# Kernel optimization log

Hardware: AMD Instinct MI355X
Metric: run time of the kernel (lower is better)

The kernel has to match this reference:

```python
import jax, jax.numpy as jnp
import numpy as np

V = 32000   # target_vocab_size
E = 512     # embedding_dim
L = 2       # enc_lstm_layers
HD = 512    # enc_lstm_hidden_dim (bidirectional encoder)
H = 2 * HD  # decoder LSTM hidden size
B = 16
T = 128
BOS = 1
CTX = L * 2 * HD          # stepwise context dim = 2048
IN0 = E + CTX             # decoder LSTM layer-0 input dim = 2560


def setup_inputs() -> dict:
    key = jax.random.key(0)
    ks = jax.random.split(key, 12)
    def w(k, shape, fan_in):
        return jax.random.normal(k, shape, jnp.float32) * np.float32(1.0 / np.sqrt(fan_in))
    return {
        "enc_lstm_hidden": jax.random.normal(ks[0], (2 * L, B, HD), jnp.float32),
        "enc_lstm_ctxt": jax.random.normal(ks[1], (2 * L, B, HD), jnp.float32),
        "minibatch_target": jax.random.randint(ks[2], (B, T), 0, V, dtype=jnp.int32),
        "emb": w(ks[3], (V, E), E),
        "w_ih_0": w(ks[4], (4 * H, IN0), IN0),
        "w_hh_0": w(ks[5], (4 * H, H), H),
        "b_ih_0": jnp.zeros((4 * H,), jnp.float32),
        "b_hh_0": jnp.zeros((4 * H,), jnp.float32),
        "w_ih_1": w(ks[6], (4 * H, H), H),
        "w_hh_1": w(ks[7], (4 * H, H), H),
        "b_ih_1": jnp.zeros((4 * H,), jnp.float32),
        "b_hh_1": jnp.zeros((4 * H,), jnp.float32),
        "fc_w": w(ks[8], (V, H), H),
        "fc_b": jnp.zeros((V,), jnp.float32),
    }


def _lstm_layer(x_seq, h0, c0, w_ih, w_hh, b):
    """x_seq: [T, B, in]; returns top outputs [T, B, H]. torch gate order i,f,g,o."""
    def step(carry, x):
        h, c = carry
        g = x @ w_ih.T + h @ w_hh.T + b
        i, f, gg, o = jnp.split(g, 4, axis=-1)
        c = jax.nn.sigmoid(f) * c + jax.nn.sigmoid(i) * jnp.tanh(gg)
        h = jax.nn.sigmoid(o) * jnp.tanh(c)
        return (h, c), h
    (hT, cT), ys = jax.lax.scan(step, (h0, c0), x_seq)
    return ys, hT, cT


def reference(enc_lstm_hidden, enc_lstm_ctxt, minibatch_target, emb,
              w_ih_0, w_hh_0, b_ih_0, b_hh_0,
              w_ih_1, w_hh_1, b_ih_1, b_hh_1, fc_w, fc_b):
    # _reshape_encoder_state: [2L,B,HD] -> [L,B,2HD] (interleave fwd/bwd per layer)
    def reshape_state(s):
        return s.reshape(L, 2, B, HD).transpose(0, 2, 1, 3).reshape(L, B, 2 * HD)
    h0 = reshape_state(enc_lstm_hidden)
    c0 = reshape_state(enc_lstm_ctxt)
    # stepwise input context: [B, 2L*HD]
    ctx = jnp.transpose(enc_lstm_hidden, (1, 0, 2)).reshape(B, CTX)
    # teacher forcing: prev tokens = [BOS, target[:, :-1]]
    tokens = jnp.concatenate(
        [jnp.full((B, 1), BOS, minibatch_target.dtype), minibatch_target[:, :-1]], axis=1)
    tok_emb = emb[tokens]                                   # [B,T,E]
    ctx_b = jnp.broadcast_to(ctx[:, None, :], (B, T, CTX))  # [B,T,CTX]
    x = jnp.concatenate([tok_emb, ctx_b], axis=-1).transpose(1, 0, 2)  # [T,B,IN0]
    x, _, _ = _lstm_layer(x, h0[0], c0[0], w_ih_0, w_hh_0, b_ih_0 + b_hh_0)
    x, _, _ = _lstm_layer(x, h0[1], c0[1], w_ih_1, w_hh_1, b_ih_1 + b_hh_1)
    out = jnp.tanh(x)                                       # [T,B,H]
    logits = jnp.einsum('tbh,vh->btv', out, fc_w) + fc_b    # [B,T,V]
    return logits
```

## Files before the change

kernel.cpp:

```cpp
#include <hip/hip_runtime.h>


#define NBLK 128

typedef float f32x4 __attribute__((ext_vector_type(4)));
typedef __bf16 bf16x8 __attribute__((ext_vector_type(8)));
typedef unsigned short u16;

__device__ __forceinline__ float sigf(float x) { return 1.0f / (1.0f + __expf(-x)); }
__device__ __forceinline__ float tanh_(float x) {
  x = fminf(15.0f, fmaxf(-15.0f, x));
  float e = __expf(2.0f * x);
  return (e - 1.0f) / (e + 1.0f);
}

__device__ __forceinline__ u16 f2bf(float f) {
  __bf16 h = (__bf16)f;
  return __builtin_bit_cast(u16, h);
}

__device__ __forceinline__ bf16x8 cvt8(float4 a, float4 b) {
  bf16x8 v;
  v[0] = (__bf16)a.x; v[1] = (__bf16)a.y; v[2] = (__bf16)a.z; v[3] = (__bf16)a.w;
  v[4] = (__bf16)b.x; v[5] = (__bf16)b.y; v[6] = (__bf16)b.z; v[7] = (__bf16)b.w;
  return v;
}

__device__ __forceinline__ void st_cv16(u16* p, u16 v) {
  unsigned vv = v;
  asm volatile("global_store_short %0, %1, off sc0 sc1" :: "v"(p), "v"(vv) : "memory");
}

__device__ __forceinline__ void flag_store(unsigned* p, unsigned v) {
  asm volatile("global_store_dword %0, %1, off sc0 sc1" :: "v"(p), "v"(v) : "memory");
}

__device__ __forceinline__ void ld2_flags(const unsigned* p0, const unsigned* p1,
                                          unsigned& a, unsigned& b) {
  asm volatile(
      "global_load_dword %0, %2, off sc0 sc1\n\t"
      "global_load_dword %1, %3, off sc0 sc1\n\t"
      "s_waitcnt vmcnt(0)"
      : "=&v"(a), "=&v"(b)
      : "v"(p0), "v"(p1)
      : "memory");
}

__device__ __forceinline__ void gsyncf(unsigned step, unsigned* bar) {
  asm volatile("s_waitcnt vmcnt(0)" ::: "memory");
  __syncthreads();
  const int tid = threadIdx.x;
  if (tid == 0) flag_store(bar + 32 + blockIdx.x * 32, step);
  if (tid < 64) {
    const unsigned* p0 = bar + 32 + tid * 64;
    const unsigned* p1 = p0 + 32;
    for (;;) {
      unsigned a, b;
      ld2_flags(p0, p1, a, b);
      if (__all((a >= step) & (b >= step))) break;
      __builtin_amdgcn_s_sleep(1);
    }
    asm volatile("" ::: "memory");
  }
  __syncthreads();
}

__device__ __forceinline__ void dot4(float& a, float4 wv, float4 xv) {
  a = fmaf(wv.x, xv.x, a);
  a = fmaf(wv.y, xv.y, a);
  a = fmaf(wv.z, xv.z, a);
  a = fmaf(wv.w, xv.w, a);
}

__global__ void prep_emb(const int* __restrict__ tgt, const float* __restrict__ emb,
                         u16* __restrict__ x0b) {
  const int g = blockIdx.x * blockDim.x + threadIdx.x;
  const int col8 = (g & 63) * 8;
  const int tb = g >> 6;
  const int t = tb >> 4, b = tb & 15;
  const int tok = (t == 0) ? 1 : tgt[b * 128 + (t - 1)];
  const float* s = emb + (size_t)tok * 512 + col8;
  float4 a = *(const float4*)s;
  float4 bb = *(const float4*)(s + 4);
  __align__(16) u16 r[8] = {f2bf(a.x), f2bf(a.y), f2bf(a.z), f2bf(a.w),
                            f2bf(bb.x), f2bf(bb.y), f2bf(bb.z), f2bf(bb.w)};
  *(uint4*)(x0b + (size_t)tb * 512 + col8) = *(uint4*)r;
}

__global__ __launch_bounds__(256, 1) void prep_ctx(const float* __restrict__ enc_h,
                                                   const float* __restrict__ wih0,
                                                   float* __restrict__ cp) {
  __shared__ float ctx[16][2052];
  const int tid = threadIdx.x;
#pragma unroll
  for (int c = 0; c < 32; ++c) {
    int f4 = tid + c * 256;
    int b = f4 >> 9, kq = f4 & 511;
    *(float4*)&ctx[b][kq * 4] =
        *(const float4*)(enc_h + (kq >> 7) * 8192 + b * 512 + (kq & 127) * 4);
  }
  __syncthreads();
  const int jr = tid >> 4, b = tid & 15;
  const int j = blockIdx.x * 16 + jr;
  const float* w = wih0 + (size_t)j * 2560 + 512;
  float a0 = 0.f, a1 = 0.f, a2 = 0.f, a3 = 0.f;
  for (int k = 0; k < 2048; k += 16) {
    float4 w0 = *(const float4*)(w + k);
    float4 w1 = *(const float4*)(w + k + 4);
    float4 w2 = *(const float4*)(w + k + 8);
    float4 w3 = *(const float4*)(w + k + 12);
    float4 x0 = *(const float4*)&ctx[b][k];
    float4 x1 = *(const float4*)&ctx[b][k + 4];
    float4 x2 = *(const float4*)&ctx[b][k + 8];
    float4 x3 = *(const float4*)&ctx[b][k + 12];
    dot4(a0, w0, x0); dot4(a1, w1, x1); dot4(a2, w2, x2); dot4(a3, w3, x3);
  }
  cp[(size_t)j * 16 + b] = a0 + a1 + a2 + a3;
}

#define BURST(ACC, BP, S, XOFF, BW)                                            \
  _Pragma("unroll")                                                            \
  for (int mm = 0; mm < 16; ++mm) {                                            \
    bf16x8 av = *(const bf16x8*)&(BP)[fr * (S) + (XOFF) + mm * 32 + ks8];      \
    ACC = __builtin_amdgcn_mfma_f32_16x16x32_bf16(av, (BW)[mm], ACC, 0, 0, 0); \
  }

__device__ __forceinline__ void loadw(bf16x8* dst, int q, int w8, int lane,
                                      const float* wih0, const float* whh0,
                                      const float* wih1, const float* whh1) {
  const int c = q >> 1, tile = q & 1;
  const int nn = lane & 15;
  const int gate = tile * 2 + (nn >> 3);
  const int unit = nn & 7;
  const int j = gate * 1024 + w8 + unit;
  const float* src;
  size_t stride = 1024;
  int ko = 0;
  if (c == 0) { src = wih0; stride = 2560; ko = 0; }
  else if (c <= 2) { src = whh0; ko = (c - 1) * 512; }
  else if (c <= 4) { src = wih1; ko = (c - 3) * 512; }
  else { src = whh1; ko = (c - 5) * 512; }
  const float* base = src + (size_t)j * stride + ko + ((lane >> 4) * 8);
#pragma unroll
  for (int mm = 0; mm < 16; ++mm) {
    const float* sp = base + mm * 32;
    dst[mm] = cvt8(*(const float4*)sp, *(const float4*)(sp + 4));
  }
}

__global__ __launch_bounds__(512, 2) void dec_seq_rw2(
    const float* __restrict__ enc_h, const float* __restrict__ enc_c,
    const float* __restrict__ wih0, const float* __restrict__ whh0,
    const float* __restrict__ wih1, const float* __restrict__ whh1,
    const float* __restrict__ bih0, const float* __restrict__ bhh0,
    const float* __restrict__ bih1, const float* __restrict__ bhh1,
    const float* __restrict__ cp, const u16* __restrict__ x0b,
    u16* __restrict__ xr, u16* __restrict__ h1r,
    u16* __restrict__ out2b, unsigned* bar) {
  __shared__ u16 xe[16 * 520];
  __shared__ u16 xs[16 * 1032];
  __shared__ u16 h1s[16 * 1032];
  __shared__ float gls[14][16][17];

  const int tid = threadIdx.x;
  const int wgid = blockIdx.x;
  const int w8 = wgid * 8;
  const int lane = tid & 63;
  const int wave = tid >> 6;
  const int fr = lane & 15;
  const int ks8 = (lane >> 4) * 8;
  unsigned step = 0;

  bf16x8 bw0[16], bw1[16];
  const int q0 = (wave < 6) ? 2 * wave : (wave == 6 ? 12 : 13);
  loadw(bw0, q0, w8, lane, wih0, whh0, wih1, whh1);
  if (wave < 6) loadw(bw1, 2 * wave + 1, w8, lane, wih0, whh0, wih1, whh1);
  else {
#pragma unroll
    for (int mm = 0; mm < 16; ++mm) bw1[mm] = bf16x8{};
  }

  const int gdj = (tid >> 4) & 7;
  const int gb = tid & 15;
  float cpA0 = 0.f, cpA1 = 0.f, cpA2 = 0.f, cpA3 = 0.f;
  float cpB0 = 0.f, cpB1 = 0.f, cpB2 = 0.f, cpB3 = 0.f;
  float c0r = 0.f, c1r = 0.f;
  if (tid < 128) {
    const int jp = w8 + gdj;
    cpA0 = cp[(size_t)(jp) * 16 + gb] + bih0[jp] + bhh0[jp];
    cpA1 = cp[(size_t)(1024 + jp) * 16 + gb] + bih0[1024 + jp] + bhh0[1024 + jp];
    cpA2 = cp[(size_t)(2048 + jp) * 16 + gb] + bih0[2048 + jp] + bhh0[2048 + jp];
    cpA3 = cp[(size_t)(3072 + jp) * 16 + gb] + bih0[3072 + jp] + bhh0[3072 + jp];
    cpB0 = bih1[jp] + bhh1[jp];
    cpB1 = bih1[1024 + jp] + bhh1[1024 + jp];
    cpB2 = bih1[2048 + jp] + bhh1[2048 + jp];
    cpB3 = bih1[3072 + jp] + bhh1[3072 + jp];
    const int dir = jp >> 9, e = jp & 511;
    c0r = enc_c[dir * 8192 + gb * 512 + e];
    c1r = enc_c[(2 + dir) * 8192 + gb * 512 + e];
    st_cv16(xr + gb * 1024 + jp, f2bf(enc_h[dir * 8192 + gb * 512 + e]));
    st_cv16(h1r + gb * 1024 + jp, f2bf(enc_h[(2 + dir) * 8192 + gb * 512 + e]));
  }

  const int sm = tid >> 5;
  const int skq = (tid & 31) * 8;

  {
    const u16* se = x0b + sm * 512;
#pragma unroll
    for (int jj = 0; jj < 2; ++jj)
      *(uint4*)&xe[sm * 520 + skq + jj * 256] = *(const uint4*)(se + skq + jj * 256);
  }
  gsyncf(++step, bar);

  for (int s = 0; s < 129; ++s) {
    const bool doA = (s < 128), doB = (s >= 1);

    uint4 rx[4], rh[4] = {}, re[2] = {};
    {
      const u16* sx = xr + (size_t)s * 16384 + sm * 1024;
#pragma unroll
      for (int jj = 0; jj < 4; ++jj) rx[jj] = *(const uint4*)(sx + skq + jj * 256);
      if (doB) {
        const u16* sh = h1r + (size_t)(s - 1) * 16384 + sm * 1024;
#pragma unroll
        for (int jj = 0; jj < 4; ++jj) rh[jj] = *(const uint4*)(sh + skq + jj * 256);
      }
      if (s < 127) {
        const u16* se = x0b + (size_t)(s + 1) * 8192 + sm * 512;
#pragma unroll
        for (int jj = 0; jj < 2; ++jj) re[jj] = *(const uint4*)(se + skq + jj * 256);
      }
    }
#pragma unroll
    for (int jj = 0; jj < 4; ++jj) *(uint4*)&xs[sm * 1032 + skq + jj * 256] = rx[jj];
    if (doB) {
#pragma unroll
      for (int jj = 0; jj < 4; ++jj) *(uint4*)&h1s[sm * 1032 + skq + jj * 256] = rh[jj];
    }
    __syncthreads();

    f32x4 acc0 = {0.f, 0.f, 0.f, 0.f}, acc1 = {0.f, 0.f, 0.f, 0.f};
    bool act0 = false, act1 = false;
    if (wave == 0) { if (doA) { BURST(acc0, xe, 520, 0, bw0) BURST(acc1, xe, 520, 0, bw1) act0 = act1 = true; } }
    else if (wave == 1) { if (doA) { BURST(acc0, xs, 1032, 0, bw0) BURST(acc1, xs, 1032, 0, bw1) act0 = act1 = true; } }
    else if (wave == 2) { if (doA) { BURST(acc0, xs, 1032, 512, bw0) BURST(acc1, xs, 1032, 512, bw1) act0 = act1 = true; } }
    else if (wave == 3) { if (doB) { BURST(acc0, xs, 1032, 0, bw0) BURST(acc1, xs, 1032, 0, bw1) act0 = act1 = true; } }
    else if (wave == 4) { if (doB) { BURST(acc0, xs, 1032, 512, bw0) BURST(acc1, xs, 1032, 512, bw1) act0 = act1 = true; } }
    else if (wave == 5) { if (doB) { BURST(acc0, h1s, 1032, 0, bw0) BURST(acc1, h1s, 1032, 0, bw1) act0 = act1 = true; } }
    else if (wave == 6) { if (doB) { BURST(acc0, h1s, 1032, 512, bw0) act0 = true; } }
    else { if (doB) { BURST(acc0, h1s, 1032, 512, bw0) act0 = true; } }
    if (act0) {
#pragma unroll
      for (int r = 0; r < 4; ++r) gls[q0][fr][(lane >> 4) * 4 + r] = acc0[r];
    }
    if (act1) {
#pragma unroll
      for (int r = 0; r < 4; ++r) gls[q0 + 1][fr][(lane >> 4) * 4 + r] = acc1[r];
    }
    __syncthreads();

    if (s < 127) {
#pragma unroll
      for (int jj = 0; jj < 2; ++jj) *(uint4*)&xe[sm * 520 + skq + jj * 256] = re[jj];
    }

    if (tid < 128) {
      const int jp = w8 + gdj;
      if (doA) {
        float gi = gls[0][gdj][gb] + gls[2][gdj][gb] + gls[4][gdj][gb] + cpA0;
        float gf = gls[0][8 + gdj][gb] + gls[2][8 + gdj][gb] + gls[4][8 + gdj][gb] + cpA1;
        float gg = gls[1][gdj][gb] + gls[3][gdj][gb] + gls[5][gdj][gb] + cpA2;
        float go = gls[1][8 + gdj][gb] + gls[3][8 + gdj][gb] + gls[5][8 + gdj][gb] + cpA3;
        c0r = sigf(gf) * c0r + sigf(gi) * tanh_(gg);
        float h = sigf(go) * tanh_(c0r);
        st_cv16(xr + (size_t)(s + 1) * 16384 + gb * 1024 + jp, f2bf(h));
      }
      if (doB) {
        float gi = gls[6][gdj][gb] + gls[8][gdj][gb] + gls[10][gdj][gb] +
                   gls[12][gdj][gb] + cpB0;
        float gf = gls[6][8 + gdj][gb] + gls[8][8 + gdj][gb] + gls[10][8 + gdj][gb] +
                   gls[12][8 + gdj][gb] + cpB1;
        float gg = gls[7][gdj][gb] + gls[9][gdj][gb] + gls[11][gdj][gb] +
                   gls[13][gdj][gb] + cpB2;
        float go = gls[7][8 + gdj][gb] + gls[9][8 + gdj][gb] + gls[11][8 + gdj][gb] +
                   gls[13][8 + gdj][gb] + cpB3;
        c1r = sigf(gf) * c1r + sigf(gi) * tanh_(gg);
        float h = sigf(go) * tanh_(c1r);
        st_cv16(h1r + (size_t)s * 16384 + gb * 1024 + jp, f2bf(h));
        out2b[((s - 1) * 16 + gb) * 1024 + jp] = f2bf(tanh_(h));
      }
    }
    gsyncf(++step, bar);
  }
}

__global__ __launch_bounds__(256, 2) void fc_gemm_mfma(
    const u16* __restrict__ A, const float* __restrict__ Bw,
    const float* __restrict__ bias, float* __restrict__ C) {
  __shared__ __align__(16) u16 Al[128][40];
  __shared__ __align__(16) u16 Bl[128][40];

  const int tid = threadIdx.x;
  const int m0 = blockIdx.x * 128;
  const int n0 = blockIdx.y * 128;
  const int wave = tid >> 6;
  const int lane = tid & 63;
  const int wm = (wave & 1) * 64;
  const int wn = (wave >> 1) * 64;
  const int fr = lane & 15;
  const int ks = lane >> 4;

  const int srow = tid >> 1;
  const int sh16 = (tid & 1) * 16;

  const u16* Ag = A + (size_t)(m0 + srow) * 1024 + sh16;
  const float* Bg = Bw + (size_t)(n0 + srow) * 1024 + sh16;

  f32x4 acc[4][4] = {};

  for (int k0 = 0; k0 < 1024; k0 += 32) {
    uint4 a0 = *(const uint4*)(Ag + k0);
    uint4 a1 = *(const uint4*)(Ag + k0 + 8);
    float bfv[16];
    *(float4*)&bfv[0] = *(const float4*)(Bg + k0);
    *(float4*)&bfv[4] = *(const float4*)(Bg + k0 + 4);
    *(float4*)&bfv[8] = *(const float4*)(Bg + k0 + 8);
    *(float4*)&bfv[12] = *(const float4*)(Bg + k0 + 12);
    u16 bu[16];
#pragma unroll
    for (int u = 0; u < 16; ++u) bu[u] = f2bf(bfv[u]);

    __syncthreads();
    *(uint4*)&Al[srow][sh16] = a0;
    *(uint4*)&Al[srow][sh16 + 8] = a1;
    *(uint4*)&Bl[srow][sh16] = *(uint4*)&bu[0];
    *(uint4*)&Bl[srow][sh16 + 8] = *(uint4*)&bu[8];
    __syncthreads();

    bf16x8 af[4], bf[4];
#pragma unroll
    for (int i = 0; i < 4; ++i) af[i] = *(const bf16x8*)&Al[wm + i * 16 + fr][ks * 8];
#pragma unroll
    for (int j = 0; j < 4; ++j) bf[j] = *(const bf16x8*)&Bl[wn + j * 16 + fr][ks * 8];
#pragma unroll
    for (int i = 0; i < 4; ++i)
#pragma unroll
      for (int j = 0; j < 4; ++j)
        acc[i][j] = __builtin_amdgcn_mfma_f32_16x16x32_bf16(af[i], bf[j], acc[i][j], 0, 0, 0);
  }

  float bj[4];
#pragma unroll
  for (int j = 0; j < 4; ++j) bj[j] = bias[n0 + wn + j * 16 + fr];

  const int mrb = (lane >> 4) * 4;
#pragma unroll
  for (int i = 0; i < 4; ++i) {
#pragma unroll
    for (int r = 0; r < 4; ++r) {
      const int m = m0 + wm + i * 16 + mrb + r;
      float* dst = C + ((size_t)(m & 15) * 128 + (m >> 4)) * 32000;
#pragma unroll
      for (int j = 0; j < 4; ++j) {
        dst[n0 + wn + j * 16 + fr] = acc[i][j][r] + bj[j];
      }
    }
  }
}

extern "C" void kernel_launch(void* const* d_in, const int* in_sizes, int n_in,
                              void* d_out, int out_size, void* d_ws, size_t ws_size,
                              hipStream_t stream) {
  const float* enc_h = (const float*)d_in[0];
  const float* enc_c = (const float*)d_in[1];
  const int* tgt = (const int*)d_in[2];
  const float* emb = (const float*)d_in[3];
  const float* wih0 = (const float*)d_in[4];
  const float* whh0 = (const float*)d_in[5];
  const float* bih0 = (const float*)d_in[6];
  const float* bhh0 = (const float*)d_in[7];
  const float* wih1 = (const float*)d_in[8];
  const float* whh1 = (const float*)d_in[9];
  const float* bih1 = (const float*)d_in[10];
  const float* bhh1 = (const float*)d_in[11];
  const float* fcw = (const float*)d_in[12];
  const float* fcb = (const float*)d_in[13];
  float* logits = (float*)d_out;

  unsigned* bar = (unsigned*)d_ws;
  hipMemsetAsync(d_ws, 0, 32768, stream);

  float* cp = (float*)((char*)d_ws + 32768);
  u16* x0b = (u16*)(cp + 65536);
  u16* xr = x0b + 1048576;
  u16* h1r = xr + 2113536;
  u16* out2b = h1r + 2113536;

  prep_emb<<<512, 256, 0, stream>>>(tgt, emb, x0b);
  prep_ctx<<<256, 256, 0, stream>>>(enc_h, wih0, cp);
  dec_seq_rw2<<<NBLK, 512, 0, stream>>>(enc_h, enc_c, wih0, whh0, wih1, whh1,
                                        bih0, bhh0, bih1, bhh1, cp, x0b,
                                        xr, h1r, out2b, bar);
  fc_gemm_mfma<<<dim3(16, 250), 256, 0, stream>>>(out2b, fcw, fcb, logits);
}
```

Before: 1.048 ms.

## Pre-convert FC weights to bf16 once per call and restructure context projection

Adds a kernel that converts fc_w to bf16 in workspace before the decoder runs. The FC GEMM then loads bf16 weights directly instead of converting fp32 in every one of the 16 M-tiles, which cuts redundant global reads and conversion work. prep_ctx is rewritten so each 16-lane group splits K and reuses each weight float4 across all 16 batch rows, followed by a shuffle reduction. The bf16 path only runs when the workspace is large enough, and the extra conversion pass adds its own traffic.

```diff
diff --git a/kernel.cpp b/kernel.cpp
--- a/kernel.cpp
+++ b/kernel.cpp
@@ -72,6 +72,15 @@
   a = fmaf(wv.w, xv.w, a);
 }
 
+__global__ void prep_bf16(const float* __restrict__ src, u16* __restrict__ dst, int n8) {
+  for (int i = blockIdx.x * blockDim.x + threadIdx.x; i < n8; i += gridDim.x * blockDim.x) {
+    float4 a = *(const float4*)(src + (size_t)i * 8);
+    float4 b = *(const float4*)(src + (size_t)i * 8 + 4);
+    bf16x8 v = cvt8(a, b);
+    *(uint4*)(dst + (size_t)i * 8) = __builtin_bit_cast(uint4, v);
+  }
+}
+
 __global__ void prep_emb(const int* __restrict__ tgt, const float* __restrict__ emb,
                          u16* __restrict__ x0b) {
   const int g = blockIdx.x * blockDim.x + threadIdx.x;
@@ -82,14 +91,13 @@
   const float* s = emb + (size_t)tok * 512 + col8;
   float4 a = *(const float4*)s;
   float4 bb = *(const float4*)(s + 4);
-  __align__(16) u16 r[8] = {f2bf(a.x), f2bf(a.y), f2bf(a.z), f2bf(a.w),
-                            f2bf(bb.x), f2bf(bb.y), f2bf(bb.z), f2bf(bb.w)};
-  *(uint4*)(x0b + (size_t)tb * 512 + col8) = *(uint4*)r;
-}
-
-__global__ __launch_bounds__(256, 1) void prep_ctx(const float* __restrict__ enc_h,
-                                                   const float* __restrict__ wih0,
-                                                   float* __restrict__ cp) {
+  bf16x8 v = cvt8(a, bb);
+  *(uint4*)(x0b + (size_t)tb * 512 + col8) = __builtin_bit_cast(uint4, v);
+}
+
+__global__ __launch_bounds__(256, 1) void prep_ctx2(const float* __restrict__ enc_h,
+                                                    const float* __restrict__ wih0,
+                                                    float* __restrict__ cp) {
   __shared__ float ctx[16][2052];
   const int tid = threadIdx.x;
 #pragma unroll
@@ -100,22 +108,22 @@
         *(const float4*)(enc_h + (kq >> 7) * 8192 + b * 512 + (kq & 127) * 4);
   }
   __syncthreads();
-  const int jr = tid >> 4, b = tid & 15;
-  const int j = blockIdx.x * 16 + jr;
+  const int r = tid >> 4, l = tid & 15;
+  const int j = blockIdx.x * 16 + r;
   const float* w = wih0 + (size_t)j * 2560 + 512;
-  float a0 = 0.f, a1 = 0.f, a2 = 0.f, a3 = 0.f;
-  for (int k = 0; k < 2048; k += 16) {
-    float4 w0 = *(const float4*)(w + k);
-    float4 w1 = *(const float4*)(w + k + 4);
-    float4 w2 = *(const float4*)(w + k + 8);
-    float4 w3 = *(const float4*)(w + k + 12);
-    float4 x0 = *(const float4*)&ctx[b][k];
-    float4 x1 = *(const float4*)&ctx[b][k + 4];
-    float4 x2 = *(const float4*)&ctx[b][k + 8];
-    float4 x3 = *(const float4*)&ctx[b][k + 12];
-    dot4(a0, w0, x0); dot4(a1, w1, x1); dot4(a2, w2, x2); dot4(a3, w3, x3);
-  }
-  cp[(size_t)j * 16 + b] = a0 + a1 + a2 + a3;
+  float acc[16] = {};
+#pragma unroll 4
+  for (int i = 0; i < 32; ++i) {
+    const int k = l * 4 + i * 64;
+    const float4 w4 = *(const float4*)(w + k);
+#pragma unroll
+    for (int b = 0; b < 16; ++b) dot4(acc[b], w4, *(const float4*)&ctx[b][k]);
+  }
+#pragma unroll
+  for (int off = 1; off < 16; off <<= 1)
+#pragma unroll
+    for (int b = 0; b < 16; ++b) acc[b] += __shfl_xor(acc[b], off);
+  cp[(size_t)j * 16 + l] = acc[l];
 }
 
 #define BURST(ACC, BP, S, XOFF, BW)                                            \
@@ -295,8 +303,8 @@
   }
 }
 
-__global__ __launch_bounds__(256, 2) void fc_gemm_mfma(
-    const u16* __restrict__ A, const float* __restrict__ Bw,
+__global__ __launch_bounds__(256, 2) void fc_gemm_bf(
+    const u16* __restrict__ A, const u16* __restrict__ Bwb,
     const float* __restrict__ bias, float* __restrict__ C) {
   __shared__ __align__(16) u16 Al[128][40];
   __shared__ __align__(16) u16 Bl[128][40];
@@ -310,15 +318,77 @@
   const int wn = (wave >> 1) * 64;
   const int fr = lane & 15;
   const int ks = lane >> 4;
-
   const int srow = tid >> 1;
   const int sh16 = (tid & 1) * 16;
 
   const u16* Ag = A + (size_t)(m0 + srow) * 1024 + sh16;
+  const u16* Bg = Bwb + (size_t)(n0 + srow) * 1024 + sh16;
+
+  f32x4 acc[4][4] = {};
+
+  for (int k0 = 0; k0 < 1024; k0 += 32) {
+    uint4 a0 = *(const uint4*)(Ag + k0);
+    uint4 a1 = *(const uint4*)(Ag + k0 + 8);
+    uint4 b0 = *(const uint4*)(Bg + k0);
+    uint4 b1 = *(const uint4*)(Bg + k0 + 8);
+
+    __syncthreads();
+    *(uint4*)&Al[srow][sh16] = a0;
+    *(uint4*)&Al[srow][sh16 + 8] = a1;
+    *(uint4*)&Bl[srow][sh16] = b0;
+    *(uint4*)&Bl[srow][sh16 + 8] = b1;
+    __syncthreads();
+
+    bf16x8 af[4], bf[4];
+#pragma unroll
+    for (int i = 0; i < 4; ++i) af[i] = *(const bf16x8*)&Al[wm + i * 16 + fr][ks * 8];
+#pragma unroll
+    for (int j = 0; j < 4; ++j) bf[j] = *(const bf16x8*)&Bl[wn + j * 16 + fr][ks * 8];
+#pragma unroll
+    for (int i = 0; i < 4; ++i)
+#pragma unroll
+      for (int j = 0; j < 4; ++j)
+        acc[i][j] = __builtin_amdgcn_mfma_f32_16x16x32_bf16(af[i], bf[j], acc[i][j], 0, 0, 0);
+  }
+
+  float bj[4];
+#pragma unroll
+  for (int j = 0; j < 4; ++j) bj[j] = bias[n0 + wn + j * 16 + fr];
+
+  const int mrb = (lane >> 4) * 4;
+#pragma unroll
+  for (int i = 0; i < 4; ++i) {
+#pragma unroll
+    for (int r = 0; r < 4; ++r) {
+      const int m = m0 + wm + i * 16 + mrb + r;
+      float* dst = C + ((size_t)(m & 15) * 128 + (m >> 4)) * 32000;
+#pragma unroll
+      for (int j = 0; j < 4; ++j) {
+        dst[n0 + wn + j * 16 + fr] = acc[i][j][r] + bj[j];
+      }
+    }
+  }
+}
+
+__global__ __launch_bounds__(256, 2) void fc_gemm_mfma(
+    const u16* __restrict__ A, const float* __restrict__ Bw,
+    const float* __restrict__ bias, float* __restrict__ C) {
+  __shared__ __align__(16) u16 Al[128][40];
+  __shared__ __align__(16) u16 Bl[128][40];
+  const int tid = threadIdx.x;
+  const int m0 = blockIdx.x * 128;
+  const int n0 = blockIdx.y * 128;
+  const int wave = tid >> 6;
+  const int lane = tid & 63;
+  const int wm = (wave & 1) * 64;
+  const int wn = (wave >> 1) * 64;
+  const int fr = lane & 15;
+  const int ks = lane >> 4;
+  const int srow = tid >> 1;
+  const int sh16 = (tid & 1) * 16;
+  const u16* Ag = A + (size_t)(m0 + srow) * 1024 + sh16;
   const float* Bg = Bw + (size_t)(n0 + srow) * 1024 + sh16;
-
   f32x4 acc[4][4] = {};
-
   for (int k0 = 0; k0 < 1024; k0 += 32) {
     uint4 a0 = *(const uint4*)(Ag + k0);
     uint4 a1 = *(const uint4*)(Ag + k0 + 8);
@@ -330,14 +400,12 @@
     u16 bu[16];
 #pragma unroll
     for (int u = 0; u < 16; ++u) bu[u] = f2bf(bfv[u]);
-
     __syncthreads();
     *(uint4*)&Al[srow][sh16] = a0;
     *(uint4*)&Al[srow][sh16 + 8] = a1;
     *(uint4*)&Bl[srow][sh16] = *(uint4*)&bu[0];
     *(uint4*)&Bl[srow][sh16 + 8] = *(uint4*)&bu[8];
     __syncthreads();
-
     bf16x8 af[4], bf[4];
 #pragma unroll
     for (int i = 0; i < 4; ++i) af[i] = *(const bf16x8*)&Al[wm + i * 16 + fr][ks * 8];
@@ -349,11 +417,9 @@
       for (int j = 0; j < 4; ++j)
         acc[i][j] = __builtin_amdgcn_mfma_f32_16x16x32_bf16(af[i], bf[j], acc[i][j], 0, 0, 0);
   }
-
   float bj[4];
 #pragma unroll
   for (int j = 0; j < 4; ++j) bj[j] = bias[n0 + wn + j * 16 + fr];
-
   const int mrb = (lane >> 4) * 4;
 #pragma unroll
   for (int i = 0; i < 4; ++i) {
@@ -362,9 +428,7 @@
       const int m = m0 + wm + i * 16 + mrb + r;
       float* dst = C + ((size_t)(m & 15) * 128 + (m >> 4)) * 32000;
 #pragma unroll
-      for (int j = 0; j < 4; ++j) {
-        dst[n0 + wn + j * 16 + fr] = acc[i][j][r] + bj[j];
-      }
+      for (int j = 0; j < 4; ++j) dst[n0 + wn + j * 16 + fr] = acc[i][j][r] + bj[j];
     }
   }
 }
@@ -396,11 +460,18 @@
   u16* xr = x0b + 1048576;
   u16* h1r = xr + 2113536;
   u16* out2b = h1r + 2113536;
+  u16* fcwb = out2b + 2097152;
+  const bool use_bf_fc = (ws_size >= 80576512ull);
 
   prep_emb<<<512, 256, 0, stream>>>(tgt, emb, x0b);
-  prep_ctx<<<256, 256, 0, stream>>>(enc_h, wih0, cp);
+  prep_ctx2<<<256, 256, 0, stream>>>(enc_h, wih0, cp);
+  if (use_bf_fc)
+    prep_bf16<<<2048, 256, 0, stream>>>(fcw, fcwb, 4096000);
   dec_seq_rw2<<<NBLK, 512, 0, stream>>>(enc_h, enc_c, wih0, whh0, wih1, whh1,
                                         bih0, bhh0, bih1, bhh1, cp, x0b,
                                         xr, h1r, out2b, bar);
-  fc_gemm_mfma<<<dim3(16, 250), 256, 0, stream>>>(out2b, fcw, fcb, logits);
-}
+  if (use_bf_fc)
+    fc_gemm_bf<<<dim3(16, 250), 256, 0, stream>>>(out2b, fcwb, fcb, logits);
+  else
+    fc_gemm_mfma<<<dim3(16, 250), 256, 0, stream>>>(out2b, fcw, fcb, logits);
+}
```

Measured after the change: 990.5 us. 5.5% less time.
